# Performance work log

Hardware: AMD Instinct MI355X
Metric: run time of the kernel (lower is better)

## Reference

```python
import jax, jax.numpy as jnp
import numpy as np

N = 50257   # vocab size
D = 128     # embedding_dim
B = 2048    # batch
C = 10      # context window size


def setup_inputs() -> dict:
    key = jax.random.key(0)
    ks = jax.random.split(key, 16)
    s = 0.02
    return {
        "x_batch": jax.random.randint(ks[0], (B,), 0, N),
        "context_words_batch": jax.random.randint(ks[1], (B, C), 0, N),
        "eps": jax.random.normal(ks[2], (B, D), dtype=jnp.float32),
        # learned parameters
        "inf_emb": jax.random.normal(ks[3], (N, D), dtype=jnp.float32) * s,
        "W_aff": jax.random.normal(ks[4], (D, 2 * D), dtype=jnp.float32) * s,
        "b_aff": jnp.zeros((D,), dtype=jnp.float32),
        "W_mu": jax.random.normal(ks[5], (D, D), dtype=jnp.float32) * s,
        "b_mu": jnp.zeros((D,), dtype=jnp.float32),
        "W_sig": jax.random.normal(ks[6], (D, D), dtype=jnp.float32) * s,
        "b_sig": jnp.zeros((D,), dtype=jnp.float32),
        "gen_sigma_emb": jax.random.normal(ks[7], (N, D), dtype=jnp.float32) * s,
        "W_gen": jax.random.normal(ks[8], (N, D), dtype=jnp.float32) * s,
        "b_gen": jnp.zeros((N,), dtype=jnp.float32),
    }


def reference(x_batch, context_words_batch, eps, inf_emb, W_aff, b_aff,
              W_mu, b_mu, W_sig, b_sig, gen_sigma_emb, W_gen, b_gen):
    # ---- inference network (vectorized over batch and context) ----
    center = inf_emb[x_batch]                    # [B, D]
    ctx = inf_emb[context_words_batch]           # [B, C, D]
    center_rep = jnp.broadcast_to(center[:, None, :], ctx.shape)  # [B, C, D]
    cat = jnp.concatenate([center_rep, ctx], axis=-1)             # [B, C, 2D]
    h = jax.nn.relu(jnp.einsum("bce,de->bcd", cat, W_aff) + b_aff)
    h_sum = h.sum(axis=1)                        # [B, D]
    inf_mu = h_sum @ W_mu.T + b_mu               # [B, D]
    inf_sigma = jax.nn.softplus(h_sum @ W_sig.T + b_sig)

    # ---- reparameterized sample ----
    z = inf_mu + eps * inf_sigma                 # [B, D]

    # ---- generative / reconstruction term ----
    logits = z @ W_gen.T + b_gen                 # [B, N] (dominant intermediate)
    logp = jax.nn.log_softmax(logits, axis=-1)
    recon = jnp.take_along_axis(logp, context_words_batch, axis=1).sum(-1)  # [B]

    # ---- KL term (faithful to original, incl. use of generative sigma) ----
    sigma = jax.nn.softplus(gen_sigma_emb[x_batch])  # [B, D]
    kl = (jnp.log(sigma / inf_sigma)
          + (inf_sigma ** 2 + (inf_mu - sigma) ** 2) / (2.0 * sigma ** 2)
          - 0.5).sum(-1)                        # [B]

    return (kl - recon).mean()
```

## Files before the change

kernel.cpp:

```cpp
#include <hip/hip_runtime.h>
#include <float.h>
#include <math.h>

#define NV 50257
#define D 128
#define B 2048
#define C 10

#define NVPAD 50272
#define NTILES (NVPAD / 16)
#define NSTREAM 96
#define NG4 (NVPAD * D / 4)
#define LOG2E 1.44269504088896f

typedef __attribute__((ext_vector_type(8))) short short8;
typedef __attribute__((ext_vector_type(4))) float float4v;

__device__ __forceinline__ float softplus_f(float x) {
    return fmaxf(x, 0.f) + log1pf(expf(-fabsf(x)));
}

__device__ __forceinline__ short f2bf(float f) {
    unsigned u = __float_as_uint(f);
    unsigned r = (u + 0x7FFFu + ((u >> 16) & 1u)) >> 16;
    return (short)r;
}

__global__ __launch_bounds__(256) void k_convert(
    const float* __restrict__ wg, const float* __restrict__ waff,
    const float* __restrict__ wmu, const float* __restrict__ wsig,
    const float* __restrict__ b_gen,
    short* __restrict__ wg_o, short* __restrict__ waff_o,
    short* __restrict__ wmu_o, short* __restrict__ wsig_o,
    float* __restrict__ bg2, float* __restrict__ out)
{
    const int i4 = blockIdx.x * 256 + threadIdx.x;
    if (i4 == 0) out[0] = 0.f;
    if (i4 < NG4) {
        const int e0 = i4 * 4;
        short4 o;
        if (e0 < NV * D) {
            const float4 g = ((const float4*)wg)[i4];
            o.x = f2bf(g.x); o.y = f2bf(g.y); o.z = f2bf(g.z); o.w = f2bf(g.w);
        } else {
            o.x = o.y = o.z = o.w = 0;
        }
        ((short4*)wg_o)[i4] = o;
        return;
    }
    const int j = i4 - NG4;
    if (j < 16384) {
        const float4* src; short4* dst; int jj;
        if (j < 8192)       { src = (const float4*)waff; dst = (short4*)waff_o; jj = j; }
        else if (j < 12288) { src = (const float4*)wmu;  dst = (short4*)wmu_o;  jj = j - 8192; }
        else                { src = (const float4*)wsig; dst = (short4*)wsig_o; jj = j - 12288; }
        const float4 g = src[jj];
        short4 o;
        o.x = f2bf(g.x); o.y = f2bf(g.y); o.z = f2bf(g.z); o.w = f2bf(g.w);
        dst[jj] = o;
    } else {
        const int jj = j - 16384;
        if (jj < NVPAD / 4) {
            const int e0 = jj * 4;
            float4 o;
            o.x = (e0 + 0 < NV) ? b_gen[e0 + 0] * LOG2E : -INFINITY;
            o.y = (e0 + 1 < NV) ? b_gen[e0 + 1] * LOG2E : -INFINITY;
            o.z = (e0 + 2 < NV) ? b_gen[e0 + 2] * LOG2E : -INFINITY;
            o.w = (e0 + 3 < NV) ? b_gen[e0 + 3] * LOG2E : -INFINITY;
            ((float4*)bg2)[jj] = o;
        }
    }
}

__global__ __launch_bounds__(256) void k_infer1(
    const int* __restrict__ x_batch, const int* __restrict__ ctxw,
    const float* __restrict__ inf_emb,
    const short* __restrict__ waff_bf, const float* __restrict__ b_aff,
    float* __restrict__ hpart)
{
    const int b0 = blockIdx.x * 16;
    const int h = blockIdx.y;
    const int t = threadIdx.x;
    const int wv = t >> 6;
    const int lane = t & 63;
    const int col16 = lane & 15;
    const int quad = lane >> 4;

    __shared__ float hsp[4][16][132];

    const int brow = b0 + col16;
    const int cidx = x_batch[brow];

    short8 ce[4];
    #pragma unroll
    for (int ks = 0; ks < 4; ++ks) {
        const float* p = inf_emb + (size_t)cidx * D + ks * 32 + quad * 8;
        const float4 g0 = *(const float4*)p;
        const float4 g1 = *(const float4*)(p + 4);
        short8 v;
        v[0] = f2bf(g0.x); v[1] = f2bf(g0.y); v[2] = f2bf(g0.z); v[3] = f2bf(g0.w);
        v[4] = f2bf(g1.x); v[5] = f2bf(g1.y); v[6] = f2bf(g1.z); v[7] = f2bf(g1.w);
        ce[ks] = v;
    }

    float4v U[8];
    #pragma unroll
    for (int dt = 0; dt < 8; ++dt) {
        float4v acc = {0.f, 0.f, 0.f, 0.f};
        #pragma unroll
        for (int ks = 0; ks < 4; ++ks) {
            const short8 bw = *(const short8*)(waff_bf + (dt * 16 + col16) * 256 + ks * 32 + quad * 8);
            acc = __builtin_amdgcn_mfma_f32_16x16x32_bf16(ce[ks], bw, acc, 0, 0, 0);
        }
        U[dt] = acc;
    }
    float ba[8];
    #pragma unroll
    for (int dt = 0; dt < 8; ++dt) ba[dt] = b_aff[dt * 16 + col16];

    float4v H[8];
    #pragma unroll
    for (int dt = 0; dt < 8; ++dt) H[dt] = (float4v){0.f, 0.f, 0.f, 0.f};

    for (int c = h * 5 + wv; c < h * 5 + 5; c += 4) {
        const int widx = ctxw[brow * C + c];
        short8 cx[4];
        #pragma unroll
        for (int ks = 0; ks < 4; ++ks) {
            const float* p = inf_emb + (size_t)widx * D + ks * 32 + quad * 8;
            const float4 g0 = *(const float4*)p;
            const float4 g1 = *(const float4*)(p + 4);
            short8 v;
            v[0] = f2bf(g0.x); v[1] = f2bf(g0.y); v[2] = f2bf(g0.z); v[3] = f2bf(g0.w);
            v[4] = f2bf(g1.x); v[5] = f2bf(g1.y); v[6] = f2bf(g1.z); v[7] = f2bf(g1.w);
            cx[ks] = v;
        }
        #pragma unroll
        for (int dt = 0; dt < 8; ++dt) {
            float4v a = {0.f, 0.f, 0.f, 0.f};
            #pragma unroll
            for (int ks = 0; ks < 4; ++ks) {
                const short8 bw = *(const short8*)(waff_bf + (dt * 16 + col16) * 256 + 128 + ks * 32 + quad * 8);
                a = __builtin_amdgcn_mfma_f32_16x16x32_bf16(cx[ks], bw, a, 0, 0, 0);
            }
            #pragma unroll
            for (int r = 0; r < 4; ++r)
                H[dt][r] += fmaxf(U[dt][r] + a[r] + ba[dt], 0.f);
        }
    }

    #pragma unroll
    for (int dt = 0; dt < 8; ++dt)
        #pragma unroll
        for (int r = 0; r < 4; ++r)
            hsp[wv][quad * 4 + r][dt * 16 + col16] = H[dt][r];
    __syncthreads();

    #pragma unroll
    for (int i = t; i < 16 * 128; i += 256) {
        const int row = i >> 7, d = i & 127;
        const float s = hsp[0][row][d] + hsp[1][row][d] + hsp[2][row][d] + hsp[3][row][d];
        hpart[((size_t)h * B + b0 + row) * D + d] = s;
    }
}

__global__ __launch_bounds__(256) void k_infer2(
    const int* __restrict__ x_batch, const float* __restrict__ eps,
    const float* __restrict__ hpart,
    const short* __restrict__ wmu_bf, const float* __restrict__ b_mu,
    const short* __restrict__ wsig_bf, const float* __restrict__ b_sig,
    const float* __restrict__ gen_sig_emb,
    float* __restrict__ z_out, short* __restrict__ zb_out,
    float* __restrict__ kl_out)
{
    const int b0 = blockIdx.x * 16;
    const int t = threadIdx.x;
    const int wv = t >> 6;
    const int lane = t & 63;
    const int col16 = lane & 15;
    const int quad = lane >> 4;

    __shared__ float kl_s[4][16];

    short8 ha[4];
    #pragma unroll
    for (int ks = 0; ks < 4; ++ks) {
        const int off = ks * 32 + quad * 8;
        const float* p0 = hpart + ((size_t)b0 + col16) * D + off;
        const float* p1 = p0 + (size_t)B * D;
        const float4 a0 = *(const float4*)p0;
        const float4 a1 = *(const float4*)(p0 + 4);
        const float4 b0v = *(const float4*)p1;
        const float4 b1v = *(const float4*)(p1 + 4);
        short8 v;
        v[0] = f2bf(a0.x + b0v.x); v[1] = f2bf(a0.y + b0v.y);
        v[2] = f2bf(a0.z + b0v.z); v[3] = f2bf(a0.w + b0v.w);
        v[4] = f2bf(a1.x + b1v.x); v[5] = f2bf(a1.y + b1v.y);
        v[6] = f2bf(a1.z + b1v.z); v[7] = f2bf(a1.w + b1v.w);
        ha[ks] = v;
    }

    int xb2[4];
    #pragma unroll
    for (int r = 0; r < 4; ++r) xb2[r] = x_batch[b0 + quad * 4 + r];

    float klp[4] = {0.f, 0.f, 0.f, 0.f};
    #pragma unroll
    for (int p = 0; p < 2; ++p) {
        const int nt = wv * 2 + p;
        float4v mu4 = {0.f, 0.f, 0.f, 0.f};
        float4v sg4 = {0.f, 0.f, 0.f, 0.f};
        #pragma unroll
        for (int ks = 0; ks < 4; ++ks) {
            const short8 bm = *(const short8*)(wmu_bf + (nt * 16 + col16) * 128 + ks * 32 + quad * 8);
            const short8 bs = *(const short8*)(wsig_bf + (nt * 16 + col16) * 128 + ks * 32 + quad * 8);
            mu4 = __builtin_amdgcn_mfma_f32_16x16x32_bf16(ha[ks], bm, mu4, 0, 0, 0);
            sg4 = __builtin_amdgcn_mfma_f32_16x16x32_bf16(ha[ks], bs, sg4, 0, 0, 0);
        }
        const int d = nt * 16 + col16;
        const float bmu = b_mu[d];
        const float bsg = b_sig[d];
        #pragma unroll
        for (int r = 0; r < 4; ++r) {
            const int b = b0 + quad * 4 + r;
            const float mu = mu4[r] + bmu;
            const float sg = sg4[r] + bsg;
            const float isig = softplus_f(sg);
            const float e = eps[b * D + d];
            const float zz = fmaf(e, isig, mu);
            z_out[b * D + d] = zz;
            zb_out[b * D + d] = f2bf(zz * LOG2E);
            const float gs = softplus_f(gen_sig_emb[(size_t)xb2[r] * D + d]);
            const float diff = mu - gs;
            klp[r] += logf(gs / isig) + (isig * isig + diff * diff) / (2.f * gs * gs) - 0.5f;
        }
    }
    #pragma unroll
    for (int off = 1; off < 16; off <<= 1)
        #pragma unroll
        for (int r = 0; r < 4; ++r)
            klp[r] += __shfl_xor(klp[r], off, 64);
    if (col16 == 0) {
        #pragma unroll
        for (int r = 0; r < 4; ++r)
            kl_s[wv][quad * 4 + r] = klp[r];
    }
    __syncthreads();
    if (t < 16) kl_out[b0 + t] = kl_s[0][t] + kl_s[1][t] + kl_s[2][t] + kl_s[3][t];
}

#define LOADP(bf, g, T) { \
    const int tt_ = ((T) < NTILES) ? (T) : 0; \
    const short* wp_ = wb + (size_t)(tt_ * 16 + col16) * D + quad * 8; \
    bf[0] = *(const short8*)(wp_); \
    bf[1] = *(const short8*)(wp_ + 32); \
    bf[2] = *(const short8*)(wp_ + 64); \
    bf[3] = *(const short8*)(wp_ + 96); \
    g = ((T) < NTILES) ? bg2t[tt_ * 16 + col16] : -INFINITY; }

#define COMP(bf, g) { \
    _Pragma("unroll") \
    for (int rt = 0; rt < 4; ++rt) { \
        float4v c = {0.f, 0.f, 0.f, 0.f}; \
        _Pragma("unroll") \
        for (int ks = 0; ks < 4; ++ks) \
            c = __builtin_amdgcn_mfma_f32_16x16x32_bf16(afrag[rt][ks], bf[ks], c, 0, 0, 0); \
        _Pragma("unroll") \
        for (int r = 0; r < 4; ++r) \
            sums[rt][r] += __builtin_amdgcn_exp2f(c[r] + g); \
    } }

__global__ __launch_bounds__(256) void k_lse_mfma(
    const short* __restrict__ zb, const short* __restrict__ wb,
    const float* __restrict__ bg2t, float* __restrict__ part_s)
{
    const int bid = blockIdx.x;
    const int s = bid % 96;
    const int x = bid / 96;
    const int t = threadIdx.x;
    const int wv = t >> 6;
    const int lane = t & 63;
    const int col16 = lane & 15;
    const int quad = lane >> 4;
    const int rowbase = x * 256 + wv * 64;

    short8 afrag[4][4];
    #pragma unroll
    for (int rt = 0; rt < 4; ++rt)
        #pragma unroll
        for (int ks = 0; ks < 4; ++ks)
            afrag[rt][ks] = *(const short8*)(zb + (rowbase + rt * 16 + col16) * D
                                                + ks * 32 + quad * 8);

    float sums[4][4];
    #pragma unroll
    for (int rt = 0; rt < 4; ++rt)
        #pragma unroll
        for (int r = 0; r < 4; ++r) sums[rt][r] = 0.f;

    short8 bA[4], bB[4], bC[4], bD[4];
    float gA, gB, gC, gD;
    LOADP(bA, gA, s);
    LOADP(bB, gB, s + 96);
    #pragma unroll 1
    for (int p = 0; p < 16; p += 2) {
        int base = s + (p + 1) * 192;
        LOADP(bC, gC, base); LOADP(bD, gD, base + 96);
        COMP(bA, gA); COMP(bB, gB);
        base = s + (p + 2) * 192;
        LOADP(bA, gA, base); LOADP(bB, gB, base + 96);
        COMP(bC, gC); COMP(bD, gD);
    }
    COMP(bA, gA); COMP(bB, gB);

    #pragma unroll
    for (int off = 1; off < 16; off <<= 1)
        #pragma unroll
        for (int rt = 0; rt < 4; ++rt)
            #pragma unroll
            for (int r = 0; r < 4; ++r)
                sums[rt][r] += __shfl_xor(sums[rt][r], off, 64);

    if (col16 == 0) {
        #pragma unroll
        for (int rt = 0; rt < 4; ++rt)
            #pragma unroll
            for (int r = 0; r < 4; ++r) {
                const int row = rowbase + rt * 16 + quad * 4 + r;
                part_s[row * NSTREAM + s] = sums[rt][r];
            }
    }
}

__global__ __launch_bounds__(256) void k_final(
    const float* __restrict__ z, const short* __restrict__ wb,
    const float* __restrict__ b_gen, const int* __restrict__ ctxw,
    const float* __restrict__ part_s, const float* __restrict__ kl,
    float* __restrict__ out)
{
    const int t = threadIdx.x;
    const int wv = t >> 6;
    const int lane = t & 63;
    __shared__ float red[4];

    float wsum = 0.f;
    #pragma unroll
    for (int rr = 0; rr < 2; ++rr) {
        const int b = blockIdx.x * 8 + wv * 2 + rr;

        int idxs[C];
        #pragma unroll
        for (int c = 0; c < C; ++c) idxs[c] = ctxw[b * C + c];
        unsigned uw[C];
        #pragma unroll
        for (int c = 0; c < C; ++c)
            uw[c] = ((const unsigned*)(wb + (size_t)idxs[c] * D))[lane];
        float sum_bg = 0.f;
        #pragma unroll
        for (int c = 0; c < C; ++c) sum_bg += b_gen[idxs[c]];

        float sv = part_s[b * NSTREAM + lane];
        if (lane < 32) sv += part_s[b * NSTREAM + 64 + lane];
        const float z0 = z[b * D + lane * 2];
        const float z1 = z[b * D + lane * 2 + 1];

        float acc = 0.f;
        #pragma unroll
        for (int c = 0; c < C; ++c) {
            const float w0 = __uint_as_float(uw[c] << 16);
            const float w1 = __uint_as_float(uw[c] & 0xFFFF0000u);
            acc = fmaf(z0, w0, acc);
            acc = fmaf(z1, w1, acc);
        }
        #pragma unroll
        for (int off = 32; off > 0; off >>= 1) {
            sv  += __shfl_xor(sv, off, 64);
            acc += __shfl_xor(acc, off, 64);
        }
        if (lane == 0) {
            const float lse = logf(sv);
            const float recon = acc + sum_bg - C * lse;
            wsum += kl[b] - recon;
        }
    }
    if (lane == 0) red[wv] = wsum;
    __syncthreads();
    if (t == 0) atomicAdd(out, (red[0] + red[1] + red[2] + red[3]) * (1.f / B));
}

extern "C" void kernel_launch(void* const* d_in, const int* in_sizes, int n_in,
                              void* d_out, int out_size, void* d_ws, size_t ws_size,
                              hipStream_t stream) {
    const int* x_batch = (const int*)d_in[0];
    const int* ctxw    = (const int*)d_in[1];
    const float* eps   = (const float*)d_in[2];
    const float* inf_emb = (const float*)d_in[3];
    const float* W_aff = (const float*)d_in[4];
    const float* b_aff = (const float*)d_in[5];
    const float* W_mu  = (const float*)d_in[6];
    const float* b_mu  = (const float*)d_in[7];
    const float* W_sig = (const float*)d_in[8];
    const float* b_sig = (const float*)d_in[9];
    const float* gen_sig = (const float*)d_in[10];
    const float* W_gen = (const float*)d_in[11];
    const float* b_gen = (const float*)d_in[12];
    float* out = (float*)d_out;

    char* ws = (char*)d_ws;
    float* z      = (float*)ws;   ws += (size_t)B * D * 4;
    float* part_s = (float*)ws;   ws += (size_t)B * NSTREAM * 4;
    float* kl     = (float*)ws;   ws += (size_t)B * 4;
    float* bg2    = (float*)ws;   ws += (size_t)NVPAD * 4;
    float* hpart  = (float*)ws;   ws += (size_t)2 * B * D * 4;
    short* z_bf   = (short*)ws;   ws += (size_t)B * D * 2;
    short* w_bf   = (short*)ws;   ws += (size_t)NVPAD * D * 2;
    short* waff_bf = (short*)ws;  ws += (size_t)128 * 256 * 2;
    short* wmu_bf  = (short*)ws;  ws += (size_t)128 * 128 * 2;
    short* wsig_bf = (short*)ws;  ws += (size_t)128 * 128 * 2;

    const int conv_items = NG4 + 16384 + NVPAD / 4;
    hipLaunchKernelGGL(k_convert, dim3((conv_items + 255) / 256), dim3(256), 0, stream,
                       W_gen, W_aff, W_mu, W_sig, b_gen,
                       w_bf, waff_bf, wmu_bf, wsig_bf, bg2, out);
    hipLaunchKernelGGL(k_infer1, dim3(B / 16, 2), dim3(256), 0, stream,
                       x_batch, ctxw, inf_emb, waff_bf, b_aff, hpart);
    hipLaunchKernelGGL(k_infer2, dim3(B / 16), dim3(256), 0, stream,
                       x_batch, eps, hpart, wmu_bf, b_mu, wsig_bf, b_sig,
                       gen_sig, z, z_bf, kl);
    hipLaunchKernelGGL(k_lse_mfma, dim3(8 * NSTREAM), dim3(256), 0, stream,
                       z_bf, w_bf, bg2, part_s);
    hipLaunchKernelGGL(k_final, dim3(B / 8), dim3(256), 0, stream,
                       z, w_bf, b_gen, ctxw, part_s, kl, out);
}
```

Before: 211.3 us.

## Fuse inference kernels into one 512-thread block and retune LSE streaming

Merges the two inference kernels into a single 8-wave kernel that reduces the per-context hidden sums in shared memory. This removes the hpart global round trip and one launch. The LSE kernel moves from 96 to 128 streams with a simpler double buffer, folds the bias into the MFMA accumulator init, and adds an occupancy hint. The fused kernel uses more shared memory, and its waves get uneven context work (2 vs 1).

```diff
diff --git a/kernel.cpp b/kernel.cpp
--- a/kernel.cpp
+++ b/kernel.cpp
@@ -9,7 +9,7 @@
 
 #define NVPAD 50272
 #define NTILES (NVPAD / 16)
-#define NSTREAM 96
+#define NSTREAM 128
 #define NG4 (NVPAD * D / 4)
 #define LOG2E 1.44269504088896f
 
@@ -72,101 +72,10 @@
     }
 }
 
-__global__ __launch_bounds__(256) void k_infer1(
+__global__ __launch_bounds__(512) void k_infer(
     const int* __restrict__ x_batch, const int* __restrict__ ctxw,
-    const float* __restrict__ inf_emb,
+    const float* __restrict__ eps, const float* __restrict__ inf_emb,
     const short* __restrict__ waff_bf, const float* __restrict__ b_aff,
-    float* __restrict__ hpart)
-{
-    const int b0 = blockIdx.x * 16;
-    const int h = blockIdx.y;
-    const int t = threadIdx.x;
-    const int wv = t >> 6;
-    const int lane = t & 63;
-    const int col16 = lane & 15;
-    const int quad = lane >> 4;
-
-    __shared__ float hsp[4][16][132];
-
-    const int brow = b0 + col16;
-    const int cidx = x_batch[brow];
-
-    short8 ce[4];
-    #pragma unroll
-    for (int ks = 0; ks < 4; ++ks) {
-        const float* p = inf_emb + (size_t)cidx * D + ks * 32 + quad * 8;
-        const float4 g0 = *(const float4*)p;
-        const float4 g1 = *(const float4*)(p + 4);
-        short8 v;
-        v[0] = f2bf(g0.x); v[1] = f2bf(g0.y); v[2] = f2bf(g0.z); v[3] = f2bf(g0.w);
-        v[4] = f2bf(g1.x); v[5] = f2bf(g1.y); v[6] = f2bf(g1.z); v[7] = f2bf(g1.w);
-        ce[ks] = v;
-    }
-
-    float4v U[8];
-    #pragma unroll
-    for (int dt = 0; dt < 8; ++dt) {
-        float4v acc = {0.f, 0.f, 0.f, 0.f};
-        #pragma unroll
-        for (int ks = 0; ks < 4; ++ks) {
-            const short8 bw = *(const short8*)(waff_bf + (dt * 16 + col16) * 256 + ks * 32 + quad * 8);
-            acc = __builtin_amdgcn_mfma_f32_16x16x32_bf16(ce[ks], bw, acc, 0, 0, 0);
-        }
-        U[dt] = acc;
-    }
-    float ba[8];
-    #pragma unroll
-    for (int dt = 0; dt < 8; ++dt) ba[dt] = b_aff[dt * 16 + col16];
-
-    float4v H[8];
-    #pragma unroll
-    for (int dt = 0; dt < 8; ++dt) H[dt] = (float4v){0.f, 0.f, 0.f, 0.f};
-
-    for (int c = h * 5 + wv; c < h * 5 + 5; c += 4) {
-        const int widx = ctxw[brow * C + c];
-        short8 cx[4];
-        #pragma unroll
-        for (int ks = 0; ks < 4; ++ks) {
-            const float* p = inf_emb + (size_t)widx * D + ks * 32 + quad * 8;
-            const float4 g0 = *(const float4*)p;
-            const float4 g1 = *(const float4*)(p + 4);
-            short8 v;
-            v[0] = f2bf(g0.x); v[1] = f2bf(g0.y); v[2] = f2bf(g0.z); v[3] = f2bf(g0.w);
-            v[4] = f2bf(g1.x); v[5] = f2bf(g1.y); v[6] = f2bf(g1.z); v[7] = f2bf(g1.w);
-            cx[ks] = v;
-        }
-        #pragma unroll
-        for (int dt = 0; dt < 8; ++dt) {
-            float4v a = {0.f, 0.f, 0.f, 0.f};
-            #pragma unroll
-            for (int ks = 0; ks < 4; ++ks) {
-                const short8 bw = *(const short8*)(waff_bf + (dt * 16 + col16) * 256 + 128 + ks * 32 + quad * 8);
-                a = __builtin_amdgcn_mfma_f32_16x16x32_bf16(cx[ks], bw, a, 0, 0, 0);
-            }
-            #pragma unroll
-            for (int r = 0; r < 4; ++r)
-                H[dt][r] += fmaxf(U[dt][r] + a[r] + ba[dt], 0.f);
-        }
-    }
-
-    #pragma unroll
-    for (int dt = 0; dt < 8; ++dt)
-        #pragma unroll
-        for (int r = 0; r < 4; ++r)
-            hsp[wv][quad * 4 + r][dt * 16 + col16] = H[dt][r];
-    __syncthreads();
-
-    #pragma unroll
-    for (int i = t; i < 16 * 128; i += 256) {
-        const int row = i >> 7, d = i & 127;
-        const float s = hsp[0][row][d] + hsp[1][row][d] + hsp[2][row][d] + hsp[3][row][d];
-        hpart[((size_t)h * B + b0 + row) * D + d] = s;
-    }
-}
-
-__global__ __launch_bounds__(256) void k_infer2(
-    const int* __restrict__ x_batch, const float* __restrict__ eps,
-    const float* __restrict__ hpart,
     const short* __restrict__ wmu_bf, const float* __restrict__ b_mu,
     const short* __restrict__ wsig_bf, const float* __restrict__ b_sig,
     const float* __restrict__ gen_sig_emb,
@@ -180,23 +89,94 @@
     const int col16 = lane & 15;
     const int quad = lane >> 4;
 
-    __shared__ float kl_s[4][16];
+    __shared__ float hsp[8][16][132];
+    __shared__ float kl_s[8][16];
+
+    const int brow = b0 + col16;
+    const int cidx = x_batch[brow];
+
+    short8 ce[4];
+    #pragma unroll
+    for (int ks = 0; ks < 4; ++ks) {
+        const float* p = inf_emb + (size_t)cidx * D + ks * 32 + quad * 8;
+        const float4 g0 = *(const float4*)p;
+        const float4 g1 = *(const float4*)(p + 4);
+        short8 v;
+        v[0] = f2bf(g0.x); v[1] = f2bf(g0.y); v[2] = f2bf(g0.z); v[3] = f2bf(g0.w);
+        v[4] = f2bf(g1.x); v[5] = f2bf(g1.y); v[6] = f2bf(g1.z); v[7] = f2bf(g1.w);
+        ce[ks] = v;
+    }
+
+    float4v U[8];
+    #pragma unroll
+    for (int dt = 0; dt < 8; ++dt) {
+        float4v acc = {0.f, 0.f, 0.f, 0.f};
+        #pragma unroll
+        for (int ks = 0; ks < 4; ++ks) {
+            const short8 bw = *(const short8*)(waff_bf + (dt * 16 + col16) * 256 + ks * 32 + quad * 8);
+            acc = __builtin_amdgcn_mfma_f32_16x16x32_bf16(ce[ks], bw, acc, 0, 0, 0);
+        }
+        U[dt] = acc;
+    }
+    float ba[8];
+    #pragma unroll
+    for (int dt = 0; dt < 8; ++dt) ba[dt] = b_aff[dt * 16 + col16];
+
+    float4v H[8];
+    #pragma unroll
+    for (int dt = 0; dt < 8; ++dt) H[dt] = (float4v){0.f, 0.f, 0.f, 0.f};
+
+    const int nctx = (wv < 2) ? 2 : 1;
+    for (int cc = 0; cc < nctx; ++cc) {
+        const int c = wv + cc * 8;
+        const int widx = ctxw[brow * C + c];
+        short8 cx[4];
+        #pragma unroll
+        for (int ks = 0; ks < 4; ++ks) {
+            const float* p = inf_emb + (size_t)widx * D + ks * 32 + quad * 8;
+            const float4 g0 = *(const float4*)p;
+            const float4 g1 = *(const float4*)(p + 4);
+            short8 v;
+            v[0] = f2bf(g0.x); v[1] = f2bf(g0.y); v[2] = f2bf(g0.z); v[3] = f2bf(g0.w);
+            v[4] = f2bf(g1.x); v[5] = f2bf(g1.y); v[6] = f2bf(g1.z); v[7] = f2bf(g1.w);
+            cx[ks] = v;
+        }
+        #pragma unroll
+        for (int dt = 0; dt < 8; ++dt) {
+            float4v a = {0.f, 0.f, 0.f, 0.f};
+            #pragma unroll
+            for (int ks = 0; ks < 4; ++ks) {
+                const short8 bw = *(const short8*)(waff_bf + (dt * 16 + col16) * 256 + 128 + ks * 32 + quad * 8);
+                a = __builtin_amdgcn_mfma_f32_16x16x32_bf16(cx[ks], bw, a, 0, 0, 0);
+            }
+            #pragma unroll
+            for (int r = 0; r < 4; ++r)
+                H[dt][r] += fmaxf(U[dt][r] + a[r] + ba[dt], 0.f);
+        }
+    }
+
+    #pragma unroll
+    for (int dt = 0; dt < 8; ++dt)
+        #pragma unroll
+        for (int r = 0; r < 4; ++r)
+            hsp[wv][quad * 4 + r][dt * 16 + col16] = H[dt][r];
+    __syncthreads();
 
     short8 ha[4];
     #pragma unroll
     for (int ks = 0; ks < 4; ++ks) {
         const int off = ks * 32 + quad * 8;
-        const float* p0 = hpart + ((size_t)b0 + col16) * D + off;
-        const float* p1 = p0 + (size_t)B * D;
-        const float4 a0 = *(const float4*)p0;
-        const float4 a1 = *(const float4*)(p0 + 4);
-        const float4 b0v = *(const float4*)p1;
-        const float4 b1v = *(const float4*)(p1 + 4);
+        float4 s0 = {0.f, 0.f, 0.f, 0.f}, s1 = {0.f, 0.f, 0.f, 0.f};
+        #pragma unroll
+        for (int w = 0; w < 8; ++w) {
+            const float4 a0 = *(const float4*)&hsp[w][col16][off];
+            const float4 a1 = *(const float4*)&hsp[w][col16][off + 4];
+            s0.x += a0.x; s0.y += a0.y; s0.z += a0.z; s0.w += a0.w;
+            s1.x += a1.x; s1.y += a1.y; s1.z += a1.z; s1.w += a1.w;
+        }
         short8 v;
-        v[0] = f2bf(a0.x + b0v.x); v[1] = f2bf(a0.y + b0v.y);
-        v[2] = f2bf(a0.z + b0v.z); v[3] = f2bf(a0.w + b0v.w);
-        v[4] = f2bf(a1.x + b1v.x); v[5] = f2bf(a1.y + b1v.y);
-        v[6] = f2bf(a1.z + b1v.z); v[7] = f2bf(a1.w + b1v.w);
+        v[0] = f2bf(s0.x); v[1] = f2bf(s0.y); v[2] = f2bf(s0.z); v[3] = f2bf(s0.w);
+        v[4] = f2bf(s1.x); v[5] = f2bf(s1.y); v[6] = f2bf(s1.z); v[7] = f2bf(s1.w);
         ha[ks] = v;
     }
 
@@ -205,9 +185,8 @@
     for (int r = 0; r < 4; ++r) xb2[r] = x_batch[b0 + quad * 4 + r];
 
     float klp[4] = {0.f, 0.f, 0.f, 0.f};
-    #pragma unroll
-    for (int p = 0; p < 2; ++p) {
-        const int nt = wv * 2 + p;
+    {
+        const int nt = wv;
         float4v mu4 = {0.f, 0.f, 0.f, 0.f};
         float4v sg4 = {0.f, 0.f, 0.f, 0.f};
         #pragma unroll
@@ -246,37 +225,43 @@
             kl_s[wv][quad * 4 + r] = klp[r];
     }
     __syncthreads();
-    if (t < 16) kl_out[b0 + t] = kl_s[0][t] + kl_s[1][t] + kl_s[2][t] + kl_s[3][t];
-}
-
-#define LOADP(bf, g, T) { \
-    const int tt_ = ((T) < NTILES) ? (T) : 0; \
+    if (t < 16) {
+        float s = 0.f;
+        #pragma unroll
+        for (int w = 0; w < 8; ++w) s += kl_s[w][t];
+        kl_out[b0 + t] = s;
+    }
+}
+
+#define LOADT(bf, g, T) { \
+    const int v_ = (T) < NTILES; \
+    const int tt_ = v_ ? (T) : 0; \
     const short* wp_ = wb + (size_t)(tt_ * 16 + col16) * D + quad * 8; \
     bf[0] = *(const short8*)(wp_); \
     bf[1] = *(const short8*)(wp_ + 32); \
     bf[2] = *(const short8*)(wp_ + 64); \
     bf[3] = *(const short8*)(wp_ + 96); \
-    g = ((T) < NTILES) ? bg2t[tt_ * 16 + col16] : -INFINITY; }
-
-#define COMP(bf, g) { \
+    g = v_ ? bg2t[tt_ * 16 + col16] : -INFINITY; }
+
+#define COMPT(bf, g) { \
     _Pragma("unroll") \
     for (int rt = 0; rt < 4; ++rt) { \
-        float4v c = {0.f, 0.f, 0.f, 0.f}; \
+        float4v c = {g, g, g, g}; \
         _Pragma("unroll") \
         for (int ks = 0; ks < 4; ++ks) \
             c = __builtin_amdgcn_mfma_f32_16x16x32_bf16(afrag[rt][ks], bf[ks], c, 0, 0, 0); \
         _Pragma("unroll") \
         for (int r = 0; r < 4; ++r) \
-            sums[rt][r] += __builtin_amdgcn_exp2f(c[r] + g); \
+            sums[rt][r] += __builtin_amdgcn_exp2f(c[r]); \
     } }
 
-__global__ __launch_bounds__(256) void k_lse_mfma(
+__global__ __launch_bounds__(256, 4) void k_lse_mfma(
     const short* __restrict__ zb, const short* __restrict__ wb,
     const float* __restrict__ bg2t, float* __restrict__ part_s)
 {
     const int bid = blockIdx.x;
-    const int s = bid % 96;
-    const int x = bid / 96;
+    const int s = bid & 127;
+    const int x = bid >> 7;
     const int t = threadIdx.x;
     const int wv = t >> 6;
     const int lane = t & 63;
@@ -298,20 +283,17 @@
         #pragma unroll
         for (int r = 0; r < 4; ++r) sums[rt][r] = 0.f;
 
-    short8 bA[4], bB[4], bC[4], bD[4];
-    float gA, gB, gC, gD;
-    LOADP(bA, gA, s);
-    LOADP(bB, gB, s + 96);
+    short8 bA[4], bB[4];
+    float gA, gB;
+    LOADT(bA, gA, s);
     #pragma unroll 1
-    for (int p = 0; p < 16; p += 2) {
-        int base = s + (p + 1) * 192;
-        LOADP(bC, gC, base); LOADP(bD, gD, base + 96);
-        COMP(bA, gA); COMP(bB, gB);
-        base = s + (p + 2) * 192;
-        LOADP(bA, gA, base); LOADP(bB, gB, base + 96);
-        COMP(bC, gC); COMP(bD, gD);
-    }
-    COMP(bA, gA); COMP(bB, gB);
+    for (int p = 0; p < 12; ++p) {
+        LOADT(bB, gB, s + (2 * p + 1) * 128);
+        COMPT(bA, gA);
+        LOADT(bA, gA, s + (2 * p + 2) * 128);
+        COMPT(bB, gB);
+    }
+    COMPT(bA, gA);
 
     #pragma unroll
     for (int off = 1; off < 16; off <<= 1)
@@ -359,8 +341,7 @@
         #pragma unroll
         for (int c = 0; c < C; ++c) sum_bg += b_gen[idxs[c]];
 
-        float sv = part_s[b * NSTREAM + lane];
-        if (lane < 32) sv += part_s[b * NSTREAM + 64 + lane];
+        float sv = part_s[b * NSTREAM + lane] + part_s[b * NSTREAM + 64 + lane];
         const float z0 = z[b * D + lane * 2];
         const float z1 = z[b * D + lane * 2 + 1];
 
@@ -411,7 +392,6 @@
     float* part_s = (float*)ws;   ws += (size_t)B * NSTREAM * 4;
     float* kl     = (float*)ws;   ws += (size_t)B * 4;
     float* bg2    = (float*)ws;   ws += (size_t)NVPAD * 4;
-    float* hpart  = (float*)ws;   ws += (size_t)2 * B * D * 4;
     short* z_bf   = (short*)ws;   ws += (size_t)B * D * 2;
     short* w_bf   = (short*)ws;   ws += (size_t)NVPAD * D * 2;
     short* waff_bf = (short*)ws;  ws += (size_t)128 * 256 * 2;
@@ -422,11 +402,9 @@
     hipLaunchKernelGGL(k_convert, dim3((conv_items + 255) / 256), dim3(256), 0, stream,
                        W_gen, W_aff, W_mu, W_sig, b_gen,
                        w_bf, waff_bf, wmu_bf, wsig_bf, bg2, out);
-    hipLaunchKernelGGL(k_infer1, dim3(B / 16, 2), dim3(256), 0, stream,
-                       x_batch, ctxw, inf_emb, waff_bf, b_aff, hpart);
-    hipLaunchKernelGGL(k_infer2, dim3(B / 16), dim3(256), 0, stream,
-                       x_batch, eps, hpart, wmu_bf, b_mu, wsig_bf, b_sig,
-                       gen_sig, z, z_bf, kl);
+    hipLaunchKernelGGL(k_infer, dim3(B / 16), dim3(512), 0, stream,
+                       x_batch, ctxw, eps, inf_emb, waff_bf, b_aff, wmu_bf, b_mu,
+                       wsig_bf, b_sig, gen_sig, z, z_bf, kl);
     hipLaunchKernelGGL(k_lse_mfma, dim3(8 * NSTREAM), dim3(256), 0, stream,
                        z_bf, w_bf, bg2, part_s);
     hipLaunchKernelGGL(k_final, dim3(B / 8), dim3(256), 0, stream,
```

Measured after the change: 252.5 us. +19.5%, slower.
